# Kernel optimization log

Measured on AMD Instinct MI355X. Metric: run time of the kernel, lower is better.

Reference implementation:

```python
import jax, jax.numpy as jnp
import numpy as np

D_MODEL = 1024
HEADS = 16
D_K = D_MODEL // HEADS
D_FF = 4096
EPS = 1e-6


def setup_inputs() -> dict:
    key = jax.random.key(0)
    ks = jax.random.split(key, 16)
    s = 1.0 / np.sqrt(D_MODEL)
    inp = {
        'x': jax.random.normal(ks[0], (4, 2048, D_MODEL), dtype=jnp.float32),
        'Wq': jax.random.normal(ks[1], (D_MODEL, D_MODEL), dtype=jnp.float32) * s,
        'bq': jnp.zeros((D_MODEL,), jnp.float32),
        'Wk': jax.random.normal(ks[2], (D_MODEL, D_MODEL), dtype=jnp.float32) * s,
        'bk': jnp.zeros((D_MODEL,), jnp.float32),
        'Wv': jax.random.normal(ks[3], (D_MODEL, D_MODEL), dtype=jnp.float32) * s,
        'bv': jnp.zeros((D_MODEL,), jnp.float32),
        'Wo': jax.random.normal(ks[4], (D_MODEL, D_MODEL), dtype=jnp.float32) * s,
        'bo': jnp.zeros((D_MODEL,), jnp.float32),
        'alpha1': jnp.ones((D_MODEL,), jnp.float32),
        'bias1': jnp.zeros((D_MODEL,), jnp.float32),
        'alpha2': jnp.ones((D_MODEL,), jnp.float32),
        'bias2': jnp.zeros((D_MODEL,), jnp.float32),
        'W1': jax.random.normal(ks[5], (D_MODEL, D_FF), dtype=jnp.float32) * s,
        'b1': jnp.zeros((D_FF,), jnp.float32),
        'W2': jax.random.normal(ks[6], (D_FF, D_MODEL), dtype=jnp.float32) * (1.0 / np.sqrt(D_FF)),
        'b2': jnp.zeros((D_MODEL,), jnp.float32),
    }
    return inp


def _residual_norm(x, residual, alpha, bias):
    # x = x + residual; norm with mean and UNBIASED std (torch x.std default),
    # eps added to std (not variance), affine alpha/bias. Dropout = identity (eval).
    s = x + residual
    mean = jnp.mean(s, axis=-1, keepdims=True)
    std = jnp.std(s, axis=-1, keepdims=True, ddof=1)
    return alpha * (s - mean) / (std + EPS) + bias


def _forward(x, Wq, bq, Wk, bk, Wv, bv, Wo, bo, alpha1, bias1, alpha2, bias2, W1, b1, W2, b2):
    B, S, D = x.shape
    # QKV projections and head split: (B, H, S, d_k)
    def split_heads(t):
        return t.reshape(B, S, HEADS, D_K).transpose(0, 2, 1, 3)
    Q = split_heads(x @ Wq + bq)
    K = split_heads(x @ Wk + bk)
    V = split_heads(x @ Wv + bv)
    # scaled dot-product attention (no mask, no dropout in eval)
    scores = jnp.einsum('bhqd,bhkd->bhqk', Q, K) / np.sqrt(D_K)
    weights = jax.nn.softmax(scores, axis=-1)
    attn = jnp.einsum('bhqk,bhkd->bhqd', weights, V)
    concat = attn.transpose(0, 2, 1, 3).reshape(B, S, D)
    attn_out = concat @ Wo + bo
    # post-norm residual 1
    norm1 = _residual_norm(attn_out, x, alpha1, bias1)
    # FFN (dropout = identity in eval)
    ff = jax.nn.relu(norm1 @ W1 + b1) @ W2 + b2
    # post-norm residual 2
    return _residual_norm(ff, norm1, alpha2, bias2)


def reference(x, Wq, bq, Wk, bk, Wv, bv, Wo, bo, alpha1, bias1, alpha2, bias2, W1, b1, W2, b2):
    return _forward(x, Wq, bq, Wk, bk, Wv, bv, Wo, bo, alpha1, bias1, alpha2, bias2, W1, b1, W2, b2)
```

## Files before the change

kernel.cpp:

```cpp
#include <hip/hip_runtime.h>
#include <hip/hip_bf16.h>
#include <stdint.h>

typedef __attribute__((ext_vector_type(8))) short bv8;
typedef __attribute__((ext_vector_type(4))) short sv4;
typedef __attribute__((ext_vector_type(4))) float f4;

#define LDS_AS __attribute__((address_space(3)))
#define GLB_AS __attribute__((address_space(1)))

#if __has_builtin(__builtin_amdgcn_exp2f)
#define EXP2F(x) __builtin_amdgcn_exp2f(x)
#else
#define EXP2F(x) exp2f(x)
#endif

__device__ __forceinline__ void gload16(const void* g, void* l) {
  __builtin_amdgcn_global_load_lds((GLB_AS void*)(g), (LDS_AS void*)(l), 16, 0, 0);
}

__device__ __forceinline__ short f2bs(float x) {
  return __builtin_bit_cast(short, __float2bfloat16(x));
}
__device__ __forceinline__ float bs2f(short s) {
  unsigned u = ((unsigned)(unsigned short)s) << 16;
  return __builtin_bit_cast(float, u);
}

__global__ __launch_bounds__(256) void k_cvt(const float* __restrict__ in, short* __restrict__ out) {
  const int i = (blockIdx.x * 256 + threadIdx.x) * 4;
  const float4 v = *(const float4*)(in + i);
  sv4 o; o[0] = f2bs(v.x); o[1] = f2bs(v.y); o[2] = f2bs(v.z); o[3] = f2bs(v.w);
  *(sv4*)(out + i) = o;
}

__global__ __launch_bounds__(256) void k_transpose(const float* __restrict__ W, short* __restrict__ Wt,
                                                   int K, int N) {
  __shared__ float tile[32][33];
  const int tx = threadIdx.x & 31, ty = threadIdx.x >> 5;
  const int n0 = blockIdx.x * 32, k0 = blockIdx.y * 32;
#pragma unroll
  for (int i = 0; i < 32; i += 8)
    tile[ty + i][tx] = W[(size_t)(k0 + ty + i) * N + n0 + tx];
  __syncthreads();
#pragma unroll
  for (int i = 0; i < 32; i += 8)
    Wt[(size_t)(n0 + ty + i) * K + k0 + tx] = f2bs(tile[tx][ty + i]);
}

template<int EPI>
__global__ __launch_bounds__(256) void k_gemm(const short* __restrict__ A, const short* __restrict__ Bt,
                                              const float* __restrict__ bias, short* __restrict__ C,
                                              int M, int N, int K) {
  __shared__ __align__(16) short As[128 * 64];
  __shared__ __align__(16) short Bs[128 * 64];
  const int t = threadIdx.x;
  const int lane = t & 63, w = t >> 6;
  const int wm = w >> 1, wn = w & 1;
  const int lr = lane & 15, lg = lane >> 4;
  const int m0 = blockIdx.y * 128, n0 = blockIdx.x * 128;

  f4 acc[4][4] = {};

  for (int k0 = 0; k0 < K; k0 += 64) {
    __syncthreads();
#pragma unroll
    for (int i = 0; i < 4; ++i) {
      const int L = t * 16 + i * 4096;
      const int row = L >> 7;
      const int cbs = (L & 127) ^ ((row & 7) << 4);
      gload16(A + (size_t)(m0 + row) * K + k0 + (cbs >> 1), (char*)As + L);
      gload16(Bt + (size_t)(n0 + row) * K + k0 + (cbs >> 1), (char*)Bs + L);
    }
    __syncthreads();
#pragma unroll
    for (int kk = 0; kk < 2; ++kk) {
      bv8 af[4], bfr[4];
#pragma unroll
      for (int mi = 0; mi < 4; ++mi) {
        const int row = wm * 64 + mi * 16 + lr;
        const int cb = kk * 64 + lg * 16;
        af[mi] = *(const bv8*)((const char*)As + row * 128 + (cb ^ ((row & 7) << 4)));
      }
#pragma unroll
      for (int ni = 0; ni < 4; ++ni) {
        const int row = wn * 64 + ni * 16 + lr;
        const int cb = kk * 64 + lg * 16;
        bfr[ni] = *(const bv8*)((const char*)Bs + row * 128 + (cb ^ ((row & 7) << 4)));
      }
#pragma unroll
      for (int mi = 0; mi < 4; ++mi)
#pragma unroll
        for (int ni = 0; ni < 4; ++ni)
          acc[mi][ni] = __builtin_amdgcn_mfma_f32_16x16x32_bf16(af[mi], bfr[ni], acc[mi][ni], 0, 0, 0);
    }
  }

#pragma unroll
  for (int ni = 0; ni < 4; ++ni) {
    const int c = n0 + wn * 64 + ni * 16 + lr;
    const float bvs = bias[c];
#pragma unroll
    for (int mi = 0; mi < 4; ++mi) {
#pragma unroll
      for (int j = 0; j < 4; ++j) {
        const int r = m0 + wm * 64 + mi * 16 + lg * 4 + j;
        float v = acc[mi][ni][j] + bvs;
        if (EPI == 1) v = fmaxf(v, 0.f);
        size_t off;
        if (EPI == 2) {
          const int b = r >> 11, s = r & 2047, h = c >> 6, d = c & 63;
          off = ((size_t)(b * 16 + h) * 2048 + s) * 64 + d;
        } else if (EPI == 3) {
          const int b = r >> 11, s = r & 2047, h = c >> 6, d = c & 63;
          off = ((size_t)(b * 16 + h) * 64 + d) * 2048 + s;
        } else {
          off = (size_t)r * N + c;
        }
        C[off] = f2bs(v);
      }
    }
  }
}

__global__ __launch_bounds__(256) void k_attn(const short* __restrict__ Qg, const short* __restrict__ Kg,
                                              const short* __restrict__ Vtg, short* __restrict__ Oc) {
  __shared__ __align__(16) short Ks[128 * 64];
  __shared__ __align__(16) short Ps[4][32 * 64];

  const int t = threadIdx.x, lane = t & 63, w = t >> 6;
  const int lr = lane & 15, lg = lane >> 4;
  const int bid = blockIdx.x;
  const int wid = (bid & 7) * 128 + (bid >> 3);
  const int q0 = (wid & 15) * 128;
  const int bh = wid >> 4;
  const int b = bh >> 4, h = bh & 15;
  const short* Qp = Qg + (size_t)bh * 2048 * 64;
  const short* Kp = Kg + (size_t)bh * 2048 * 64;
  const short* Vp = Vtg + (size_t)bh * 64 * 2048;

  bv8 qf[2][2];
#pragma unroll
  for (int mi = 0; mi < 2; ++mi)
#pragma unroll
    for (int kk = 0; kk < 2; ++kk)
      qf[mi][kk] = *(const bv8*)(Qp + (size_t)(q0 + w * 32 + mi * 16 + lr) * 64 + kk * 32 + lg * 8);

  f4 Oa[2][4] = {};
  float mrow[2] = {-1e30f, -1e30f};
  float lsum[2] = {0.f, 0.f};
  const float SC = 0.125f * 1.44269504089f;
  short* Pw = (short*)Ps[w];

  for (int kt = 0; kt < 2048; kt += 128) {
    __syncthreads();
#pragma unroll
    for (int i = 0; i < 4; ++i) {
      const int L = t * 16 + i * 4096;
      const int row = L >> 7;
      const int cbs = (L & 127) ^ ((row & 7) << 4);
      gload16(Kp + (size_t)(kt + row) * 64 + (cbs >> 1), (char*)Ks + L);
    }
    __syncthreads();

#pragma unroll
    for (int hf = 0; hf < 2; ++hf) {
      f4 Sa[2][4] = {};
      __builtin_amdgcn_s_setprio(1);
#pragma unroll
      for (int kk = 0; kk < 2; ++kk) {
        bv8 kf[4];
#pragma unroll
        for (int nl = 0; nl < 4; ++nl) {
          const int row = (hf * 4 + nl) * 16 + lr;
          const int cb = kk * 64 + lg * 16;
          kf[nl] = *(const bv8*)((const char*)Ks + row * 128 + (cb ^ ((row & 7) << 4)));
        }
#pragma unroll
        for (int mi = 0; mi < 2; ++mi)
#pragma unroll
          for (int nl = 0; nl < 4; ++nl)
            Sa[mi][nl] = __builtin_amdgcn_mfma_f32_16x16x32_bf16(kf[nl], qf[mi][kk], Sa[mi][nl], 0, 0, 0);
      }
      __builtin_amdgcn_s_setprio(0);

#pragma unroll
      for (int mi = 0; mi < 2; ++mi) {
        float pm = Sa[mi][0][0];
#pragma unroll
        for (int nl = 0; nl < 4; ++nl)
#pragma unroll
          for (int j = 0; j < 4; ++j) pm = fmaxf(pm, Sa[mi][nl][j]);
        pm = fmaxf(pm, __shfl_xor(pm, 16));
        pm = fmaxf(pm, __shfl_xor(pm, 32));
        const float mn = fmaxf(mrow[mi], pm);
        const float scf = EXP2F((mrow[mi] - mn) * SC);
        mrow[mi] = mn;
        const float nm = -mn * SC;
        float rs = 0.f;
#pragma unroll
        for (int nl = 0; nl < 4; ++nl)
#pragma unroll
          for (int j = 0; j < 4; ++j) {
            const float p = EXP2F(fmaf(Sa[mi][nl][j], SC, nm));
            Sa[mi][nl][j] = p;
            rs += p;
          }
        rs += __shfl_xor(rs, 16);
        rs += __shfl_xor(rs, 32);
        lsum[mi] = lsum[mi] * scf + rs;
#pragma unroll
        for (int nO = 0; nO < 4; ++nO)
#pragma unroll
          for (int j = 0; j < 4; ++j) Oa[mi][nO][j] *= scf;
      }

#pragma unroll
      for (int mi = 0; mi < 2; ++mi)
#pragma unroll
        for (int nl = 0; nl < 4; ++nl) {
          const int q = mi * 16 + lr;
          const int cb = (nl * 32 + lg * 8) ^ ((q & 7) << 4);
          sv4 pk;
          pk[0] = f2bs(Sa[mi][nl][0]); pk[1] = f2bs(Sa[mi][nl][1]);
          pk[2] = f2bs(Sa[mi][nl][2]); pk[3] = f2bs(Sa[mi][nl][3]);
          *(sv4*)((char*)Pw + q * 128 + cb) = pk;
        }

#pragma unroll
      for (int k2 = 0; k2 < 2; ++k2) {
        bv8 vf[4], pf[2];
#pragma unroll
        for (int nO = 0; nO < 4; ++nO)
          vf[nO] = *(const bv8*)(Vp + (size_t)(nO * 16 + lr) * 2048 + kt + hf * 64 + k2 * 32 + lg * 8);
#pragma unroll
        for (int mi = 0; mi < 2; ++mi) {
          const int row = mi * 16 + lr;
          const int cb = (k2 * 64 + lg * 16) ^ ((row & 7) << 4);
          pf[mi] = *(const bv8*)((const char*)Pw + row * 128 + cb);
        }
        __builtin_amdgcn_s_setprio(1);
#pragma unroll
        for (int mi = 0; mi < 2; ++mi)
#pragma unroll
          for (int nO = 0; nO < 4; ++nO)
            Oa[mi][nO] = __builtin_amdgcn_mfma_f32_16x16x32_bf16(vf[nO], pf[mi], Oa[mi][nO], 0, 0, 0);
        __builtin_amdgcn_s_setprio(0);
      }
    }
  }

#pragma unroll
  for (int mi = 0; mi < 2; ++mi) {
    const float inv = 1.f / lsum[mi];
    const int q = q0 + w * 32 + mi * 16 + lr;
#pragma unroll
    for (int nO = 0; nO < 4; ++nO) {
      sv4 o;
#pragma unroll
      for (int j = 0; j < 4; ++j) o[j] = f2bs(Oa[mi][nO][j] * inv);
      const int c = h * 64 + nO * 16 + lg * 4;
      *(sv4*)(Oc + ((size_t)b * 2048 + q) * 1024 + c) = o;
    }
  }
}

template<int MODE>
__global__ __launch_bounds__(256) void k_resnorm(const short* __restrict__ a, const void* __restrict__ res,
                                                 const float* __restrict__ alpha, const float* __restrict__ beta,
                                                 void* __restrict__ out) {
  const int row = blockIdx.x;
  const int t = threadIdx.x;
  const int lane = t & 63, w = t >> 6;
  const size_t base = (size_t)row * 1024;

  const sv4 av = *(const sv4*)(a + base + t * 4);
  float v[4];
  if (MODE == 0) {
    const float4 rv = *(const float4*)((const float*)res + base + t * 4);
    v[0] = bs2f(av[0]) + rv.x; v[1] = bs2f(av[1]) + rv.y;
    v[2] = bs2f(av[2]) + rv.z; v[3] = bs2f(av[3]) + rv.w;
  } else {
    const sv4 rv = *(const sv4*)((const short*)res + base + t * 4);
#pragma unroll
    for (int i = 0; i < 4; ++i) v[i] = bs2f(av[i]) + bs2f(rv[i]);
  }
  float s = v[0] + v[1] + v[2] + v[3];
  float sq = v[0] * v[0] + v[1] * v[1] + v[2] * v[2] + v[3] * v[3];
#pragma unroll
  for (int m = 1; m < 64; m <<= 1) { s += __shfl_xor(s, m); sq += __shfl_xor(sq, m); }
  __shared__ float red[8];
  if (lane == 0) { red[w] = s; red[w + 4] = sq; }
  __syncthreads();
  s = red[0] + red[1] + red[2] + red[3];
  sq = red[4] + red[5] + red[6] + red[7];
  const float mean = s * (1.f / 1024.f);
  const float var = (sq - 1024.f * mean * mean) * (1.f / 1023.f);
  const float inv = 1.f / (sqrtf(fmaxf(var, 0.f)) + 1e-6f);
  const float4 al = *(const float4*)(alpha + t * 4);
  const float4 be = *(const float4*)(beta + t * 4);
  float y[4];
  y[0] = al.x * (v[0] - mean) * inv + be.x;
  y[1] = al.y * (v[1] - mean) * inv + be.y;
  y[2] = al.z * (v[2] - mean) * inv + be.z;
  y[3] = al.w * (v[3] - mean) * inv + be.w;
  if (MODE == 0) {
    sv4 o; o[0] = f2bs(y[0]); o[1] = f2bs(y[1]); o[2] = f2bs(y[2]); o[3] = f2bs(y[3]);
    *(sv4*)((short*)out + base + t * 4) = o;
  } else {
    *(float4*)((float*)out + base + t * 4) = make_float4(y[0], y[1], y[2], y[3]);
  }
}

extern "C" void kernel_launch(void* const* d_in, const int* in_sizes, int n_in,
                              void* d_out, int out_size, void* d_ws, size_t ws_size,
                              hipStream_t stream) {
  const float* x   = (const float*)d_in[0];
  const float* Wq  = (const float*)d_in[1];
  const float* bq  = (const float*)d_in[2];
  const float* Wk  = (const float*)d_in[3];
  const float* bk  = (const float*)d_in[4];
  const float* Wv  = (const float*)d_in[5];
  const float* bv  = (const float*)d_in[6];
  const float* Wo  = (const float*)d_in[7];
  const float* bo  = (const float*)d_in[8];
  const float* al1 = (const float*)d_in[9];
  const float* bi1 = (const float*)d_in[10];
  const float* al2 = (const float*)d_in[11];
  const float* bi2 = (const float*)d_in[12];
  const float* W1  = (const float*)d_in[13];
  const float* b1  = (const float*)d_in[14];
  const float* W2  = (const float*)d_in[15];
  const float* b2  = (const float*)d_in[16];

  if (ws_size < (size_t)136 * 1024 * 1024) return;

  char* ws = (char*)d_ws;
  short* xb  = (short*)(ws);
  short* Qb  = (short*)(ws + (16ll << 20));
  short* Kb  = (short*)(ws + (32ll << 20));
  short* Vtb = (short*)(ws + (48ll << 20));
  short* Hb  = (short*)(ws);
  short* Wqt = (short*)(ws + (64ll << 20));
  short* Wkt = (short*)(ws + (66ll << 20));
  short* Wvt = (short*)(ws + (68ll << 20));
  short* Wot = (short*)(ws + (70ll << 20));
  short* W1t = (short*)(ws + (72ll << 20));
  short* W2t = (short*)(ws + (80ll << 20));
  short* Cc  = (short*)(ws + (88ll << 20));
  short* AOb = (short*)(ws + (104ll << 20));
  short* N1b = (short*)(ws + (120ll << 20));
  short* FFb = (short*)(ws + (104ll << 20));

  k_cvt<<<8192, 256, 0, stream>>>(x, xb);
  k_transpose<<<dim3(32, 32), 256, 0, stream>>>(Wq, Wqt, 1024, 1024);
  k_transpose<<<dim3(32, 32), 256, 0, stream>>>(Wk, Wkt, 1024, 1024);
  k_transpose<<<dim3(32, 32), 256, 0, stream>>>(Wv, Wvt, 1024, 1024);
  k_transpose<<<dim3(32, 32), 256, 0, stream>>>(Wo, Wot, 1024, 1024);
  k_transpose<<<dim3(128, 32), 256, 0, stream>>>(W1, W1t, 1024, 4096);
  k_transpose<<<dim3(32, 128), 256, 0, stream>>>(W2, W2t, 4096, 1024);

  k_gemm<2><<<dim3(8, 64), 256, 0, stream>>>(xb, Wqt, bq, Qb, 8192, 1024, 1024);
  k_gemm<2><<<dim3(8, 64), 256, 0, stream>>>(xb, Wkt, bk, Kb, 8192, 1024, 1024);
  k_gemm<3><<<dim3(8, 64), 256, 0, stream>>>(xb, Wvt, bv, Vtb, 8192, 1024, 1024);

  k_attn<<<1024, 256, 0, stream>>>(Qb, Kb, Vtb, Cc);

  k_gemm<0><<<dim3(8, 64), 256, 0, stream>>>(Cc, Wot, bo, AOb, 8192, 1024, 1024);
  k_resnorm<0><<<8192, 256, 0, stream>>>(AOb, x, al1, bi1, N1b);

  k_gemm<1><<<dim3(32, 64), 256, 0, stream>>>(N1b, W1t, b1, Hb, 8192, 4096, 1024);
  k_gemm<0><<<dim3(8, 64), 256, 0, stream>>>(Hb, W2t, b2, FFb, 8192, 1024, 4096);
  k_resnorm<1><<<8192, 256, 0, stream>>>(FFb, N1b, al2, bi2, (float*)d_out);
}
```

Before: 470.9 us.

## Load K fragments directly from global and skip rescale when max barely changes

The attention kernel no longer stages K tiles in LDS behind two barriers per tile. Each wave now reads its K fragments straight from global memory (relying on L1/L2 caching) and the block-wide syncs go away. It also adds a lazy-rescale trick: when the new row max exceeds the running max by at most 8 in the log2-scaled domain, the running max is kept and the O/l rescale is skipped. The max reduction is tree-structured, and setprio now wraps only the MFMA block. The costs are redundant global traffic for K across the four waves and possibly more exposed load latency.

```diff
diff --git a/kernel.cpp b/kernel.cpp
--- a/kernel.cpp
+++ b/kernel.cpp
@@ -125,7 +125,6 @@
 
 __global__ __launch_bounds__(256) void k_attn(const short* __restrict__ Qg, const short* __restrict__ Kg,
                                               const short* __restrict__ Vtg, short* __restrict__ Oc) {
-  __shared__ __align__(16) short Ks[128 * 64];
   __shared__ __align__(16) short Ps[4][32 * 64];
 
   const int t = threadIdx.x, lane = t & 63, w = t >> 6;
@@ -153,50 +152,43 @@
   short* Pw = (short*)Ps[w];
 
   for (int kt = 0; kt < 2048; kt += 128) {
-    __syncthreads();
-#pragma unroll
-    for (int i = 0; i < 4; ++i) {
-      const int L = t * 16 + i * 4096;
-      const int row = L >> 7;
-      const int cbs = (L & 127) ^ ((row & 7) << 4);
-      gload16(Kp + (size_t)(kt + row) * 64 + (cbs >> 1), (char*)Ks + L);
-    }
-    __syncthreads();
-
 #pragma unroll
     for (int hf = 0; hf < 2; ++hf) {
       f4 Sa[2][4] = {};
-      __builtin_amdgcn_s_setprio(1);
 #pragma unroll
       for (int kk = 0; kk < 2; ++kk) {
         bv8 kf[4];
 #pragma unroll
-        for (int nl = 0; nl < 4; ++nl) {
-          const int row = (hf * 4 + nl) * 16 + lr;
-          const int cb = kk * 64 + lg * 16;
-          kf[nl] = *(const bv8*)((const char*)Ks + row * 128 + (cb ^ ((row & 7) << 4)));
-        }
+        for (int nl = 0; nl < 4; ++nl)
+          kf[nl] = *(const bv8*)(Kp + (size_t)(kt + (hf * 4 + nl) * 16 + lr) * 64 + kk * 32 + lg * 8);
+        __builtin_amdgcn_s_setprio(1);
 #pragma unroll
         for (int mi = 0; mi < 2; ++mi)
 #pragma unroll
           for (int nl = 0; nl < 4; ++nl)
             Sa[mi][nl] = __builtin_amdgcn_mfma_f32_16x16x32_bf16(kf[nl], qf[mi][kk], Sa[mi][nl], 0, 0, 0);
-      }
-      __builtin_amdgcn_s_setprio(0);
+        __builtin_amdgcn_s_setprio(0);
+      }
 
 #pragma unroll
       for (int mi = 0; mi < 2; ++mi) {
-        float pm = Sa[mi][0][0];
-#pragma unroll
-        for (int nl = 0; nl < 4; ++nl)
-#pragma unroll
-          for (int j = 0; j < 4; ++j) pm = fmaxf(pm, Sa[mi][nl][j]);
+        float a0 = fmaxf(fmaxf(Sa[mi][0][0], Sa[mi][0][1]), fmaxf(Sa[mi][0][2], Sa[mi][0][3]));
+        float a1 = fmaxf(fmaxf(Sa[mi][1][0], Sa[mi][1][1]), fmaxf(Sa[mi][1][2], Sa[mi][1][3]));
+        float a2 = fmaxf(fmaxf(Sa[mi][2][0], Sa[mi][2][1]), fmaxf(Sa[mi][2][2], Sa[mi][2][3]));
+        float a3 = fmaxf(fmaxf(Sa[mi][3][0], Sa[mi][3][1]), fmaxf(Sa[mi][3][2], Sa[mi][3][3]));
+        float pm = fmaxf(fmaxf(a0, a1), fmaxf(a2, a3));
         pm = fmaxf(pm, __shfl_xor(pm, 16));
         pm = fmaxf(pm, __shfl_xor(pm, 32));
-        const float mn = fmaxf(mrow[mi], pm);
-        const float scf = EXP2F((mrow[mi] - mn) * SC);
-        mrow[mi] = mn;
-        const float nm = -mn * SC;
+        const bool skip = __all((pm - mrow[mi]) * SC <= 8.f);
+        float scf;
+        if (skip) {
+          scf = 1.f;
+        } else {
+          const float mn = fmaxf(mrow[mi], pm);
+          scf = EXP2F((mrow[mi] - mn) * SC);
+          mrow[mi] = mn;
+        }
+        const float nm = -mrow[mi] * SC;
         float rs = 0.f;
 #pragma unroll
         for (int nl = 0; nl < 4; ++nl)
@@ -209,10 +201,12 @@
         rs += __shfl_xor(rs, 16);
         rs += __shfl_xor(rs, 32);
         lsum[mi] = lsum[mi] * scf + rs;
-#pragma unroll
-        for (int nO = 0; nO < 4; ++nO)
-#pragma unroll
-          for (int j = 0; j < 4; ++j) Oa[mi][nO][j] *= scf;
+        if (!skip) {
+#pragma unroll
+          for (int nO = 0; nO < 4; ++nO)
+#pragma unroll
+            for (int j = 0; j < 4; ++j) Oa[mi][nO][j] *= scf;
+        }
       }
 
 #pragma unroll
```

After: 553.0 us. +17.4%, slower.
